# Kernel optimization log

Hardware: AMD Instinct MI355X
Metric: run time of the kernel (lower is better)

Reference implementation:

```python
import jax, jax.numpy as jnp
import numpy as np

ADAPTER_RATIO = 0.2


def setup_inputs() -> dict:
    key = jax.random.key(0)
    k1, k2, k3, k4, k5 = jax.random.split(key, 5)
    B, C, H, D = 16384, 512, 128, 3  # batch, feature dim, bottleneck, n_domains
    n_text = (D + 1) * 345           # original + 3 domain prompt sets, 345 classes
    return {
        "image_features": jax.random.normal(k1, (B, C), dtype=jnp.float32),
        "domain_label": jax.random.randint(k2, (B,), 0, D),
        "W1": jax.random.normal(k3, (D, C, H), dtype=jnp.float32) * 0.02,
        "W2": jax.random.normal(k4, (D, H, C), dtype=jnp.float32) * 0.02,
        "text_features": jax.random.normal(k5, (n_text, C), dtype=jnp.float32),
        "logit_scale": jnp.ones((1,), dtype=jnp.float32) * jnp.log(jnp.float32(100.0)),
    }


def reference(image_features, domain_label, W1, W2, text_features, logit_scale):
    # Per-sample routed adapters: run all D tiny adapters densely, then gather
    # each sample's routed output (equivalent to torch per-sample dispatch loop).
    h = jax.nn.relu(jnp.einsum("bi,dij->dbj", image_features, W1))   # [D,B,H]
    a = jax.nn.relu(jnp.einsum("dbj,djk->dbk", h, W2))                # [D,B,C]
    adapter_features = jnp.take_along_axis(
        a, domain_label[None, :, None], axis=0)[0]                     # [B,C]
    feats = ADAPTER_RATIO * adapter_features + (1.0 - ADAPTER_RATIO) * image_features
    feats = feats / jnp.linalg.norm(feats, axis=-1, keepdims=True)
    # text features are pre-normalized in the original module
    txt = text_features / jnp.linalg.norm(text_features, axis=-1, keepdims=True)
    logits = jnp.exp(logit_scale[0]) * (feats @ txt.T)                 # [B, n_text]
    return logits
```

## Files before the change

kernel.cpp:

```cpp
#include <hip/hip_runtime.h>
#include <math.h>

typedef __bf16 bf16;
typedef __attribute__((ext_vector_type(8))) __bf16 bf16x8;
typedef __attribute__((ext_vector_type(4))) __bf16 bf16x4;
typedef __attribute__((ext_vector_type(4))) float f32x4;

#define MFMA(a, b, c) __builtin_amdgcn_mfma_f32_16x16x32_bf16((a), (b), (c), 0, 0, 0)
#define BARR() __builtin_amdgcn_s_barrier()
#define SFEN() __builtin_amdgcn_sched_barrier(0)
#define WAITV(n) asm volatile("s_waitcnt vmcnt(" #n ")" ::: "memory")
#define LGKM0() asm volatile("s_waitcnt lgkmcnt(0)" ::: "memory")

static constexpr int NB = 16384;
static constexpr int NC = 512;
static constexpr int NH = 128;
static constexpr int ND = 3;
static constexpr int NT = 1380;
static constexpr int NTP = 1408;
static constexpr int NTILE = 131;
static constexpr int NPMAX = NTILE * 128;

__device__ __forceinline__ void gld16(const bf16* g, void* l) {
  __builtin_amdgcn_global_load_lds(
      (const __attribute__((address_space(1))) void*)g,
      (__attribute__((address_space(3))) void*)l, 16, 0, 0);
}

__global__ __launch_bounds__(64) void k_prep(
    const float* __restrict__ W1, const float* __restrict__ W2,
    const float* __restrict__ txt,
    bf16* __restrict__ W1t, bf16* __restrict__ W2t, bf16* __restrict__ Tbf)
{
  __shared__ float tl[64][65];
  const int b = blockIdx.x, t = threadIdx.x;
  if (b < NTP) {
    bf16x4* dst = (bf16x4*)(Tbf + (size_t)b * NC);
    if (b < NT) {
      const float4* src = (const float4*)(txt + (size_t)b * NC);
      float4 u0 = src[t * 2], u1 = src[t * 2 + 1];
      float ssq = u0.x * u0.x + u0.y * u0.y + u0.z * u0.z + u0.w * u0.w +
                  u1.x * u1.x + u1.y * u1.y + u1.z * u1.z + u1.w * u1.w;
      for (int m = 32; m; m >>= 1) ssq += __shfl_xor(ssq, m, 64);
      float inv = 1.0f / sqrtf(ssq);
      bf16x4 o0 = {(bf16)(u0.x * inv), (bf16)(u0.y * inv), (bf16)(u0.z * inv), (bf16)(u0.w * inv)};
      bf16x4 o1 = {(bf16)(u1.x * inv), (bf16)(u1.y * inv), (bf16)(u1.z * inv), (bf16)(u1.w * inv)};
      dst[t * 2] = o0; dst[t * 2 + 1] = o1;
    } else {
      bf16x4 z = {(bf16)0.f, (bf16)0.f, (bf16)0.f, (bf16)0.f};
      dst[t * 2] = z; dst[t * 2 + 1] = z;
    }
  } else if (b < NTP + 48) {
    const int e = b - NTP, d = e >> 4, rem = e & 15;
    const int i0 = (rem >> 1) * 64, n0 = (rem & 1) * 64;
    const float* src = W1 + (size_t)d * NC * NH;
    for (int r = 0; r < 64; ++r) tl[r][t] = src[(size_t)(i0 + r) * NH + n0 + t];
    __syncthreads();
    bf16* dst = W1t + (size_t)d * NH * NC;
    for (int r = 0; r < 64; ++r)
      dst[(size_t)(n0 + r) * NC + i0 + t] = (bf16)tl[t][r];
  } else {
    const int e = b - (NTP + 48), d = e >> 4, rem = e & 15;
    const int j0 = (rem >> 3) * 64, n0 = (rem & 7) * 64;
    const float* src = W2 + (size_t)d * NH * NC;
    for (int r = 0; r < 64; ++r) tl[r][t] = src[(size_t)(j0 + r) * NC + n0 + t];
    __syncthreads();
    bf16* dst = W2t + (size_t)d * NC * NH;
    for (int r = 0; r < 64; ++r)
      dst[(size_t)(n0 + r) * NH + j0 + t] = (bf16)tl[t][r];
  }
}

__global__ __launch_bounds__(1024) void k_sort(
    const int* __restrict__ lab, int* __restrict__ map, int* __restrict__ dmeta)
{
  __shared__ int woff[16][3];
  __shared__ int segbase[4];
  __shared__ int padded[3];
  const int t = threadIdx.x, lane = t & 63, wv = t >> 6;
  int c[3] = {0, 0, 0};
  int ld[16];
  const int base = t * 16;
#pragma unroll
  for (int i = 0; i < 16; ++i) { ld[i] = lab[base + i]; c[ld[i]]++; }
  int exc[3];
#pragma unroll
  for (int d = 0; d < 3; ++d) {
    int v = c[d];
    for (int off = 1; off < 64; off <<= 1) {
      int u = __shfl_up(v, off, 64);
      if (lane >= off) v += u;
    }
    exc[d] = v - c[d];
    if (lane == 63) woff[wv][d] = v;
  }
  __syncthreads();
  if (t == 0) {
    int tot[3] = {0, 0, 0};
    for (int w = 0; w < 16; ++w)
      for (int d = 0; d < 3; ++d) { int v = woff[w][d]; woff[w][d] = tot[d]; tot[d] += v; }
    int s = 0;
    for (int d = 0; d < 3; ++d) {
      padded[d] = (tot[d] + 127) & ~127;
      segbase[d] = s; s += padded[d];
    }
    segbase[3] = s;
    dmeta[NTILE] = s;
  }
  __syncthreads();
  for (int tile = t; tile < NTILE; tile += 1024) {
    const int slot = tile * 128;
    int dd = -1;
    for (int d = 0; d < 3; ++d)
      if (slot >= segbase[d] && slot < segbase[d] + padded[d]) dd = d;
    dmeta[tile] = dd;
  }
  for (int i = t; i < NPMAX; i += 1024) map[i] = -1;
  __syncthreads();
  int pos[3];
#pragma unroll
  for (int d = 0; d < 3; ++d) pos[d] = segbase[d] + woff[wv][d] + exc[d];
#pragma unroll
  for (int i = 0; i < 16; ++i) { int d = ld[i]; map[pos[d]++] = base + i; }
}

__global__ __launch_bounds__(512) void k_adapter(
    const float* __restrict__ X, const bf16* __restrict__ W1t,
    const bf16* __restrict__ W2t, const int* __restrict__ map,
    const int* __restrict__ dmeta, bf16* __restrict__ Fbf)
{
  __shared__ bf16 As[2][64 * 64];
  __shared__ bf16 Hs[64 * 128];
  __shared__ float rssq[8][64];
  __shared__ int smap[64];
  const int bx = blockIdx.x;
  const int d = dmeta[bx >> 1];
  if (d < 0) return;
  const int t = threadIdx.x, w = t >> 6, l = t & 63;
  const int lr = l & 15, lg = l >> 4;
  const int row0 = bx * 64;
  if (t < 64) smap[t] = map[row0 + t];

  int arow = map[row0 + (t >> 3)]; if (arow < 0) arow = 0;
  const float4* Xr = (const float4*)(X + (size_t)arow * NC);
  const int f4b = (t & 7) * 2;
  const int wrow = t >> 3;
  const int wcb = ((t & 7) * 16) ^ ((wrow & 7) << 4);

  float4 R0a, R0b, R1a, R1b;
#define LOADR0(kt) { R0a = Xr[(kt) * 16 + f4b]; R0b = Xr[(kt) * 16 + f4b + 1]; }
#define LOADR1(kt) { R1a = Xr[(kt) * 16 + f4b]; R1b = Xr[(kt) * 16 + f4b + 1]; }
#define CVTW(buf, Ra, Rb) {                                                   \
    bf16x8 v_;                                                                \
    v_[0] = (bf16)Ra.x; v_[1] = (bf16)Ra.y; v_[2] = (bf16)Ra.z;               \
    v_[3] = (bf16)Ra.w; v_[4] = (bf16)Rb.x; v_[5] = (bf16)Rb.y;               \
    v_[6] = (bf16)Rb.z; v_[7] = (bf16)Rb.w;                                   \
    *(bf16x8*)((char*)As[buf] + wrow * 128 + wcb) = v_; }

  f32x4 acc1[4] = {};
  const bf16* W1B = W1t + (size_t)d * NH * NC + (size_t)(w * 16 + lr) * NC;
  LOADR0(0); LOADR1(1);
  CVTW(0, R0a, R0b);
  LOADR0(2);
  LGKM0(); BARR(); SFEN();
#pragma unroll 1
  for (int kt = 0; kt < 8; ++kt) {
    const int cur = kt & 1;
    if (kt + 1 < 8) {
      if (cur == 0) { CVTW(1, R1a, R1b); if (kt + 3 < 8) LOADR1(kt + 3); }
      else          { CVTW(0, R0a, R0b); if (kt + 3 < 8) LOADR0(kt + 3); }
    }
#pragma unroll
    for (int h = 0; h < 2; ++h) {
      bf16x8 a[4];
#pragma unroll
      for (int m = 0; m < 4; ++m) {
        const int r = m * 16 + lr;
        a[m] = *(const bf16x8*)((const char*)As[cur] +
                                r * 128 + ((h * 64 + lg * 16) ^ ((r & 7) << 4)));
      }
      const bf16x8 bq = *(const bf16x8*)(W1B + kt * 64 + h * 32 + lg * 8);
#pragma unroll
      for (int m = 0; m < 4; ++m) acc1[m] = MFMA(a[m], bq, acc1[m]);
    }
    LGKM0(); SFEN(); BARR(); SFEN();
  }
#undef LOADR0
#undef LOADR1
#undef CVTW

#pragma unroll
  for (int m = 0; m < 4; ++m)
#pragma unroll
    for (int r = 0; r < 4; ++r) {
      const int row = m * 16 + lg * 4 + r;
      const int colb = (w * 16 + lr) * 2;
      const float v = acc1[m][r];
      *(bf16*)((char*)Hs + row * 256 + (colb ^ ((row & 7) << 4))) =
          (bf16)(v > 0.f ? v : 0.f);
    }
  __syncthreads();

  f32x4 acc[4][4] = {};
  const bf16* W2B = W2t + (size_t)d * NC * NH + (size_t)(w * 64) * NH;
#pragma unroll
  for (int ks = 0; ks < 4; ++ks) {
    bf16x8 a[4], bq[4];
#pragma unroll
    for (int m = 0; m < 4; ++m) {
      const int r = m * 16 + lr;
      a[m] = *(const bf16x8*)((const char*)Hs +
                              r * 256 + ((ks * 64 + lg * 16) ^ ((r & 7) << 4)));
    }
#pragma unroll
    for (int n = 0; n < 4; ++n)
      bq[n] = *(const bf16x8*)(W2B + (size_t)(n * 16 + lr) * NH + ks * 32 + lg * 8);
#pragma unroll
    for (int m = 0; m < 4; ++m)
#pragma unroll
      for (int n = 0; n < 4; ++n)
        acc[m][n] = MFMA(a[m], bq[n], acc[m][n]);
  }

  const int col0 = w * 64;
#pragma unroll
  for (int m = 0; m < 4; ++m)
#pragma unroll
    for (int r = 0; r < 4; ++r) {
      const int rl = m * 16 + lg * 4 + r;
      const int grow = smap[rl];
      const size_t row = grow < 0 ? 0 : (size_t)grow;
      float part = 0.f;
#pragma unroll
      for (int n = 0; n < 4; ++n) {
        const int col = col0 + n * 16 + lr;
        float v = acc[m][n][r];
        v = v > 0.f ? v : 0.f;
        v = 0.2f * v + 0.8f * X[row * NC + col];
        acc[m][n][r] = v;
        part += v * v;
      }
      part += __shfl_xor(part, 1, 64);
      part += __shfl_xor(part, 2, 64);
      part += __shfl_xor(part, 4, 64);
      part += __shfl_xor(part, 8, 64);
      if (lr == 0) rssq[w][rl] = part;
    }
  __syncthreads();
#pragma unroll
  for (int m = 0; m < 4; ++m)
#pragma unroll
    for (int r = 0; r < 4; ++r) {
      const int rl = m * 16 + lg * 4 + r;
      const int grow = smap[rl];
      if (grow < 0) continue;
      float tot = 0.f;
#pragma unroll
      for (int ww = 0; ww < 8; ++ww) tot += rssq[ww][rl];
      const float inv = 1.0f / sqrtf(tot);
#pragma unroll
      for (int n = 0; n < 4; ++n) {
        const int col = col0 + n * 16 + lr;
        Fbf[(size_t)grow * NC + col] = (bf16)(acc[m][n][r] * inv);
      }
    }
}

__global__ __launch_bounds__(256) void k_gemm3(
    const bf16* __restrict__ Fbf, const bf16* __restrict__ Tbf,
    const float* __restrict__ lsc, float* __restrict__ out)
{
  __shared__ bf16 As[2][128 * 32];
  __shared__ bf16 Bs[2][128 * 32];
  const int bx = blockIdx.x, by = blockIdx.y;
  const int t = threadIdx.x, w = t >> 6, l = t & 63;
  const int wr = w >> 1, wc = w & 1;
  const int lr = l & 15, lg = l >> 4;
  const int row0 = bx * 128, col0 = by * 128;
  const bf16* Ag = Fbf + (size_t)row0 * NC;
  const bf16* Bg = Tbf + (size_t)col0 * NC;

#define STG3(buf, kt)                                                         \
  {                                                                           \
    _Pragma("unroll")                                                         \
    for (int i = 0; i < 2; ++i) {                                             \
      const int off = (i * 256 + t) * 16;                                     \
      const int row = off >> 6;                                               \
      const int src = (off & 63) ^ (((row >> 1) & 3) << 4);                   \
      const size_t go = (size_t)row * NC + (size_t)(kt) * 32 + (src >> 1);    \
      gld16(Ag + go, (char*)As[buf] + off);                                   \
      gld16(Bg + go, (char*)Bs[buf] + off);                                   \
    }                                                                         \
  }

  f32x4 acc[4][4] = {};
  STG3(0, 0);
#pragma unroll 1
  for (int ks = 0; ks < 16; ++ks) {
    const int cur = ks & 1;
    __syncthreads();
    if (ks + 1 < 16) STG3(cur ^ 1, ks + 1);
    bf16x8 a[4], b[4];
#pragma unroll
    for (int m = 0; m < 4; ++m) {
      const int r = wr * 64 + m * 16 + lr;
      a[m] = *(const bf16x8*)&As[cur][r * 32 + ((lg * 8) ^ (((r >> 1) & 3) << 3))];
    }
#pragma unroll
    for (int n = 0; n < 4; ++n) {
      const int r = wc * 64 + n * 16 + lr;
      b[n] = *(const bf16x8*)&Bs[cur][r * 32 + ((lg * 8) ^ (((r >> 1) & 3) << 3))];
    }
#pragma unroll
    for (int m = 0; m < 4; ++m)
#pragma unroll
      for (int n = 0; n < 4; ++n)
        acc[m][n] = MFMA(a[m], b[n], acc[m][n]);
  }

  const float s = expf(lsc[0]);
#pragma unroll
  for (int m = 0; m < 4; ++m)
#pragma unroll
    for (int n = 0; n < 4; ++n)
#pragma unroll
      for (int r = 0; r < 4; ++r) {
        const int row = row0 + wr * 64 + m * 16 + lg * 4 + r;
        const int col = col0 + wc * 64 + n * 16 + lr;
        if (col < NT) out[(size_t)row * NT + col] = s * acc[m][n][r];
      }
#undef STG3
}

extern "C" void kernel_launch(void* const* d_in, const int* in_sizes, int n_in,
                              void* d_out, int out_size, void* d_ws, size_t ws_size,
                              hipStream_t stream) {
  const float* X   = (const float*)d_in[0];
  const int*   lab = (const int*)d_in[1];
  const float* W1  = (const float*)d_in[2];
  const float* W2  = (const float*)d_in[3];
  const float* txt = (const float*)d_in[4];
  const float* lsc = (const float*)d_in[5];
  float* out = (float*)d_out;

  char* ws = (char*)d_ws;
  constexpr size_t SZ_W1T = (size_t)ND * NH * NC * 2;
  constexpr size_t SZ_W2T = (size_t)ND * NC * NH * 2;
  constexpr size_t SZ_TBF = (size_t)NTP * NC * 2;
  constexpr size_t SZ_FBF = (size_t)NB * NC * 2;
  constexpr size_t SZ_MAP = (size_t)NPMAX * 4;
  bf16* W1t = (bf16*)(ws);
  bf16* W2t = (bf16*)(ws + SZ_W1T);
  bf16* Tbf = (bf16*)(ws + SZ_W1T + SZ_W2T);
  bf16* Fbf = (bf16*)(ws + SZ_W1T + SZ_W2T + SZ_TBF);
  int*  map = (int*)(ws + SZ_W1T + SZ_W2T + SZ_TBF + SZ_FBF);
  int*  dmeta = (int*)(ws + SZ_W1T + SZ_W2T + SZ_TBF + SZ_FBF + SZ_MAP);

  k_prep<<<NTP + 96, 64, 0, stream>>>(W1, W2, txt, W1t, W2t, Tbf);
  k_sort<<<1, 1024, 0, stream>>>(lab, map, dmeta);
  k_adapter<<<2 * NTILE, 512, 0, stream>>>(X, W1t, W2t, map, dmeta, Fbf);
  k_gemm3<<<dim3(NB / 128, NTP / 128), 256, 0, stream>>>(Fbf, Tbf, lsc, out);
}
```

Baseline: 92.75 us.

## Fuse prep and sort kernels, keep bf16 X tiles in LDS for residual

Merges the weight/text preparation kernel and the label sorting kernel into one 1024-thread launch, and rewrites the text-normalisation and weight-transpose paths to use wider blocks with vectorised loads and stores. In the adapter kernel, all eight converted X k-tiles now stay in LDS, so the residual term reads them back instead of issuing a second global fp32 load of X. This removes one kernel launch and a global read pass. The cost is more LDS per block, which may lower occupancy, and the residual now uses bf16-rounded X instead of fp32, which slightly reduces precision.

```diff
diff --git a/kernel.cpp b/kernel.cpp
--- a/kernel.cpp
+++ b/kernel.cpp
@@ -27,101 +27,107 @@
       (__attribute__((address_space(3))) void*)l, 16, 0, 0);
 }
 
-__global__ __launch_bounds__(64) void k_prep(
+__global__ __launch_bounds__(1024) void k_prep(
     const float* __restrict__ W1, const float* __restrict__ W2,
-    const float* __restrict__ txt,
-    bf16* __restrict__ W1t, bf16* __restrict__ W2t, bf16* __restrict__ Tbf)
+    const float* __restrict__ txt, const int* __restrict__ lab,
+    bf16* __restrict__ W1t, bf16* __restrict__ W2t, bf16* __restrict__ Tbf,
+    int* __restrict__ map, int* __restrict__ dmeta)
 {
   __shared__ float tl[64][65];
+  __shared__ int woff[16][3];
+  __shared__ int segbase[4];
+  __shared__ int padded[3];
   const int b = blockIdx.x, t = threadIdx.x;
-  if (b < NTP) {
-    bf16x4* dst = (bf16x4*)(Tbf + (size_t)b * NC);
-    if (b < NT) {
-      const float4* src = (const float4*)(txt + (size_t)b * NC);
-      float4 u0 = src[t * 2], u1 = src[t * 2 + 1];
+
+  if (b < 88) {
+    const int wv = t >> 6, lane = t & 63;
+    const int row = b * 16 + wv;
+    bf16x4* dst = (bf16x4*)(Tbf + (size_t)row * NC);
+    if (row < NT) {
+      const float4* src = (const float4*)(txt + (size_t)row * NC);
+      float4 u0 = src[lane * 2], u1 = src[lane * 2 + 1];
       float ssq = u0.x * u0.x + u0.y * u0.y + u0.z * u0.z + u0.w * u0.w +
                   u1.x * u1.x + u1.y * u1.y + u1.z * u1.z + u1.w * u1.w;
       for (int m = 32; m; m >>= 1) ssq += __shfl_xor(ssq, m, 64);
       float inv = 1.0f / sqrtf(ssq);
       bf16x4 o0 = {(bf16)(u0.x * inv), (bf16)(u0.y * inv), (bf16)(u0.z * inv), (bf16)(u0.w * inv)};
       bf16x4 o1 = {(bf16)(u1.x * inv), (bf16)(u1.y * inv), (bf16)(u1.z * inv), (bf16)(u1.w * inv)};
-      dst[t * 2] = o0; dst[t * 2 + 1] = o1;
+      dst[lane * 2] = o0; dst[lane * 2 + 1] = o1;
     } else {
       bf16x4 z = {(bf16)0.f, (bf16)0.f, (bf16)0.f, (bf16)0.f};
-      dst[t * 2] = z; dst[t * 2 + 1] = z;
-    }
-  } else if (b < NTP + 48) {
-    const int e = b - NTP, d = e >> 4, rem = e & 15;
+      dst[lane * 2] = z; dst[lane * 2 + 1] = z;
+    }
+  } else if (b < 136) {
+    const int e = b - 88, d = e >> 4, rem = e & 15;
     const int i0 = (rem >> 1) * 64, n0 = (rem & 1) * 64;
+    const int rr = t >> 4, c4 = (t & 15) * 4;
     const float* src = W1 + (size_t)d * NC * NH;
-    for (int r = 0; r < 64; ++r) tl[r][t] = src[(size_t)(i0 + r) * NH + n0 + t];
+    float4 v = *(const float4*)&src[(size_t)(i0 + rr) * NH + n0 + c4];
+    tl[rr][c4] = v.x; tl[rr][c4 + 1] = v.y; tl[rr][c4 + 2] = v.z; tl[rr][c4 + 3] = v.w;
     __syncthreads();
     bf16* dst = W1t + (size_t)d * NH * NC;
-    for (int r = 0; r < 64; ++r)
-      dst[(size_t)(n0 + r) * NC + i0 + t] = (bf16)tl[t][r];
+    bf16x4 o = {(bf16)tl[c4][rr], (bf16)tl[c4 + 1][rr],
+                (bf16)tl[c4 + 2][rr], (bf16)tl[c4 + 3][rr]};
+    *(bf16x4*)&dst[(size_t)(n0 + rr) * NC + i0 + c4] = o;
+  } else if (b < 184) {
+    const int e = b - 136, d = e >> 4, rem = e & 15;
+    const int j0 = (rem >> 3) * 64, n0 = (rem & 7) * 64;
+    const int rr = t >> 4, c4 = (t & 15) * 4;
+    const float* src = W2 + (size_t)d * NH * NC;
+    float4 v = *(const float4*)&src[(size_t)(j0 + rr) * NC + n0 + c4];
+    tl[rr][c4] = v.x; tl[rr][c4 + 1] = v.y; tl[rr][c4 + 2] = v.z; tl[rr][c4 + 3] = v.w;
+    __syncthreads();
+    bf16* dst = W2t + (size_t)d * NC * NH;
+    bf16x4 o = {(bf16)tl[c4][rr], (bf16)tl[c4 + 1][rr],
+                (bf16)tl[c4 + 2][rr], (bf16)tl[c4 + 3][rr]};
+    *(bf16x4*)&dst[(size_t)(n0 + rr) * NH + j0 + c4] = o;
   } else {
-    const int e = b - (NTP + 48), d = e >> 4, rem = e & 15;
-    const int j0 = (rem >> 3) * 64, n0 = (rem & 7) * 64;
-    const float* src = W2 + (size_t)d * NH * NC;
-    for (int r = 0; r < 64; ++r) tl[r][t] = src[(size_t)(j0 + r) * NC + n0 + t];
-    __syncthreads();
-    bf16* dst = W2t + (size_t)d * NC * NH;
-    for (int r = 0; r < 64; ++r)
-      dst[(size_t)(n0 + r) * NH + j0 + t] = (bf16)tl[t][r];
-  }
-}
-
-__global__ __launch_bounds__(1024) void k_sort(
-    const int* __restrict__ lab, int* __restrict__ map, int* __restrict__ dmeta)
-{
-  __shared__ int woff[16][3];
-  __shared__ int segbase[4];
-  __shared__ int padded[3];
-  const int t = threadIdx.x, lane = t & 63, wv = t >> 6;
-  int c[3] = {0, 0, 0};
-  int ld[16];
-  const int base = t * 16;
-#pragma unroll
-  for (int i = 0; i < 16; ++i) { ld[i] = lab[base + i]; c[ld[i]]++; }
-  int exc[3];
-#pragma unroll
-  for (int d = 0; d < 3; ++d) {
-    int v = c[d];
-    for (int off = 1; off < 64; off <<= 1) {
-      int u = __shfl_up(v, off, 64);
-      if (lane >= off) v += u;
-    }
-    exc[d] = v - c[d];
-    if (lane == 63) woff[wv][d] = v;
-  }
-  __syncthreads();
-  if (t == 0) {
-    int tot[3] = {0, 0, 0};
-    for (int w = 0; w < 16; ++w)
-      for (int d = 0; d < 3; ++d) { int v = woff[w][d]; woff[w][d] = tot[d]; tot[d] += v; }
-    int s = 0;
+    const int lane = t & 63, wv = t >> 6;
+    int c[3] = {0, 0, 0};
+    int ld[16];
+    const int base = t * 16;
+#pragma unroll
+    for (int i = 0; i < 16; ++i) { ld[i] = lab[base + i]; c[ld[i]]++; }
+    int exc[3];
+#pragma unroll
     for (int d = 0; d < 3; ++d) {
-      padded[d] = (tot[d] + 127) & ~127;
-      segbase[d] = s; s += padded[d];
-    }
-    segbase[3] = s;
-    dmeta[NTILE] = s;
-  }
-  __syncthreads();
-  for (int tile = t; tile < NTILE; tile += 1024) {
-    const int slot = tile * 128;
-    int dd = -1;
-    for (int d = 0; d < 3; ++d)
-      if (slot >= segbase[d] && slot < segbase[d] + padded[d]) dd = d;
-    dmeta[tile] = dd;
-  }
-  for (int i = t; i < NPMAX; i += 1024) map[i] = -1;
-  __syncthreads();
-  int pos[3];
-#pragma unroll
-  for (int d = 0; d < 3; ++d) pos[d] = segbase[d] + woff[wv][d] + exc[d];
-#pragma unroll
-  for (int i = 0; i < 16; ++i) { int d = ld[i]; map[pos[d]++] = base + i; }
+      int v = c[d];
+      for (int off = 1; off < 64; off <<= 1) {
+        int u = __shfl_up(v, off, 64);
+        if (lane >= off) v += u;
+      }
+      exc[d] = v - c[d];
+      if (lane == 63) woff[wv][d] = v;
+    }
+    __syncthreads();
+    if (t == 0) {
+      int tot[3] = {0, 0, 0};
+      for (int w = 0; w < 16; ++w)
+        for (int d = 0; d < 3; ++d) { int v = woff[w][d]; woff[w][d] = tot[d]; tot[d] += v; }
+      int s = 0;
+      for (int d = 0; d < 3; ++d) {
+        padded[d] = (tot[d] + 127) & ~127;
+        segbase[d] = s; s += padded[d];
+      }
+      segbase[3] = s;
+      dmeta[NTILE] = s;
+    }
+    __syncthreads();
+    for (int tile = t; tile < NTILE; tile += 1024) {
+      const int slot = tile * 128;
+      int dd = -1;
+      for (int d = 0; d < 3; ++d)
+        if (slot >= segbase[d] && slot < segbase[d] + padded[d]) dd = d;
+      dmeta[tile] = dd;
+    }
+    for (int i = t; i < NPMAX; i += 1024) map[i] = -1;
+    __syncthreads();
+    int pos[3];
+#pragma unroll
+    for (int d = 0; d < 3; ++d) pos[d] = segbase[d] + woff[wv][d] + exc[d];
+#pragma unroll
+    for (int i = 0; i < 16; ++i) { int d = ld[i]; map[pos[d]++] = base + i; }
+  }
 }
 
 __global__ __launch_bounds__(512) void k_adapter(
@@ -129,7 +135,7 @@
     const bf16* __restrict__ W2t, const int* __restrict__ map,
     const int* __restrict__ dmeta, bf16* __restrict__ Fbf)
 {
-  __shared__ bf16 As[2][64 * 64];
+  __shared__ bf16 As[8][64 * 64];
   __shared__ bf16 Hs[64 * 128];
   __shared__ float rssq[8][64];
   __shared__ int smap[64];
@@ -150,12 +156,12 @@
   float4 R0a, R0b, R1a, R1b;
 #define LOADR0(kt) { R0a = Xr[(kt) * 16 + f4b]; R0b = Xr[(kt) * 16 + f4b + 1]; }
 #define LOADR1(kt) { R1a = Xr[(kt) * 16 + f4b]; R1b = Xr[(kt) * 16 + f4b + 1]; }
-#define CVTW(buf, Ra, Rb) {                                                   \
+#define CVTW(kt, Ra, Rb) {                                                    \
     bf16x8 v_;                                                                \
     v_[0] = (bf16)Ra.x; v_[1] = (bf16)Ra.y; v_[2] = (bf16)Ra.z;               \
     v_[3] = (bf16)Ra.w; v_[4] = (bf16)Rb.x; v_[5] = (bf16)Rb.y;               \
     v_[6] = (bf16)Rb.z; v_[7] = (bf16)Rb.w;                                   \
-    *(bf16x8*)((char*)As[buf] + wrow * 128 + wcb) = v_; }
+    *(bf16x8*)((char*)As[kt] + wrow * 128 + wcb) = v_; }
 
   f32x4 acc1[4] = {};
   const bf16* W1B = W1t + (size_t)d * NH * NC + (size_t)(w * 16 + lr) * NC;
@@ -165,10 +171,9 @@
   LGKM0(); BARR(); SFEN();
 #pragma unroll 1
   for (int kt = 0; kt < 8; ++kt) {
-    const int cur = kt & 1;
     if (kt + 1 < 8) {
-      if (cur == 0) { CVTW(1, R1a, R1b); if (kt + 3 < 8) LOADR1(kt + 3); }
-      else          { CVTW(0, R0a, R0b); if (kt + 3 < 8) LOADR0(kt + 3); }
+      if ((kt & 1) == 0) { CVTW(kt + 1, R1a, R1b); if (kt + 3 < 8) LOADR1(kt + 3); }
+      else              { CVTW(kt + 1, R0a, R0b); if (kt + 3 < 8) LOADR0(kt + 3); }
     }
 #pragma unroll
     for (int h = 0; h < 2; ++h) {
@@ -176,7 +181,7 @@
 #pragma unroll
       for (int m = 0; m < 4; ++m) {
         const int r = m * 16 + lr;
-        a[m] = *(const bf16x8*)((const char*)As[cur] +
+        a[m] = *(const bf16x8*)((const char*)As[kt] +
                                 r * 128 + ((h * 64 + lg * 16) ^ ((r & 7) << 4)));
       }
       const bf16x8 bq = *(const bf16x8*)(W1B + kt * 64 + h * 32 + lg * 8);
@@ -229,14 +234,15 @@
     for (int r = 0; r < 4; ++r) {
       const int rl = m * 16 + lg * 4 + r;
       const int grow = smap[rl];
-      const size_t row = grow < 0 ? 0 : (size_t)grow;
       float part = 0.f;
 #pragma unroll
       for (int n = 0; n < 4; ++n) {
-        const int col = col0 + n * 16 + lr;
+        const int cw = n * 16 + lr;
+        const float xv = (float)*(const bf16*)((const char*)As[w] +
+                              rl * 128 + ((cw * 2) ^ ((rl & 7) << 4)));
         float v = acc[m][n][r];
         v = v > 0.f ? v : 0.f;
-        v = 0.2f * v + 0.8f * X[row * NC + col];
+        v = 0.2f * v + 0.8f * xv;
         acc[m][n][r] = v;
         part += v * v;
       }
@@ -245,6 +251,7 @@
       part += __shfl_xor(part, 4, 64);
       part += __shfl_xor(part, 8, 64);
       if (lr == 0) rssq[w][rl] = part;
+      (void)grow;
     }
   __syncthreads();
 #pragma unroll
@@ -356,8 +363,7 @@
   int*  map = (int*)(ws + SZ_W1T + SZ_W2T + SZ_TBF + SZ_FBF);
   int*  dmeta = (int*)(ws + SZ_W1T + SZ_W2T + SZ_TBF + SZ_FBF + SZ_MAP);
 
-  k_prep<<<NTP + 96, 64, 0, stream>>>(W1, W2, txt, W1t, W2t, Tbf);
-  k_sort<<<1, 1024, 0, stream>>>(lab, map, dmeta);
+  k_prep<<<185, 1024, 0, stream>>>(W1, W2, txt, lab, W1t, W2t, Tbf, map, dmeta);
   k_adapter<<<2 * NTILE, 512, 0, stream>>>(X, W1t, W2t, map, dmeta, Fbf);
   k_gemm3<<<dim3(NB / 128, NTP / 128), 256, 0, stream>>>(Fbf, Tbf, lsc, out);
 }
```

After: 99.50 us. +7.3%, slower.
